# Kernel tuning notes

Hardware: AMD Instinct MI355X
Metric: run time of the kernel (lower is better)

The kernel has to match this reference:

```python
import jax, jax.numpy as jnp
import numpy as np

STRIDE = 1
PADDING = 1  # zeros padding mode

def setup_inputs() -> dict:
    key = jax.random.key(0)
    k1, k2, k3 = jax.random.split(key, 3)
    N, C_in, H, W = 32, 128, 56, 56
    C_out, kH, kW = 256, 3, 3
    x = jax.random.normal(k1, (N, C_in, H, W), dtype=jnp.float32)
    fan_in = C_in * kH * kW
    weight = jax.random.normal(k2, (C_out, C_in, kH, kW), dtype=jnp.float32) / np.sqrt(fan_in)
    bias = jax.random.normal(k3, (C_out,), dtype=jnp.float32) * 0.01
    return {"x": x, "weight": weight, "bias": bias}

def reference(x, weight, bias):
    # Same math as the im2col unfold + GEMM: a standard 2D cross-correlation
    # with zero padding. Expressed as the fused implicit-GEMM conv primitive.
    out = jax.lax.conv_general_dilated(
        x, weight,
        window_strides=(STRIDE, STRIDE),
        padding=[(PADDING, PADDING), (PADDING, PADDING)],
        dimension_numbers=("NCHW", "OIHW", "NCHW"),
    )
    # bias broadcast over (N, C_out, H_out, W_out)
    return out + bias[None, :, None, None]
```

## Files before the change

### kernel.cpp

```cpp
#include <hip/hip_runtime.h>


typedef __attribute__((ext_vector_type(8))) short short8;
typedef __attribute__((ext_vector_type(4))) float float4v;

constexpr int NB = 32, CI = 128, HH = 56, WW = 56, CO = 256;
constexpr int HWP = HH * WW;
constexpr int HP = 58, WP = 58;
constexpr size_t XTP_BYTES = (size_t)NB * HP * WP * CI * 2;
constexpr size_t WT_OFF    = XTP_BYTES;
constexpr size_t WT_BYTES  = (size_t)9 * CO * CI * 2;
constexpr size_t WS_NEED   = WT_OFF + WT_BYTES;

__device__ inline ushort f2bf(float v) {
    union { float f; uint u; } c; c.f = v;
    uint u = c.u;
    return (ushort)((u + 0x7fffu + ((u >> 16) & 1u)) >> 16);
}

__device__ inline void gll(const ushort* g, ushort* l) {
    __builtin_amdgcn_global_load_lds(
        (const __attribute__((address_space(1))) uint*)g,
        (__attribute__((address_space(3))) uint*)l, 16, 0, 0);
}

__global__ __launch_bounds__(256) void xform_x(const float* __restrict__ x,
                                               ushort* __restrict__ xTp) {
    int b = blockIdx.x;
    int cit = b & 3;
    int hwt = (b >> 2) % 49;
    int n   = b / (4 * 49);
    int ci0 = cit * 32, hw0 = hwt * 64;
    __shared__ float t[32][65];
    int tx = threadIdx.x;
    int col = tx & 63, r4 = tx >> 6;
#pragma unroll
    for (int rr = 0; rr < 8; ++rr) {
        int row = rr * 4 + r4;
        t[row][col] = x[((size_t)n * CI + ci0 + row) * HWP + hw0 + col];
    }
    __syncthreads();
    int i = tx & 31, j0 = tx >> 5;
#pragma unroll
    for (int jj = 0; jj < 8; ++jj) {
        int j = jj * 8 + j0;
        int hw = hw0 + j;
        int h = hw / WW, w = hw % WW;
        xTp[(((size_t)n * HP + h + 1) * WP + (w + 1)) * CI + ci0 + i] = f2bf(t[i][j]);
    }
}

__global__ __launch_bounds__(256) void xform_border(ushort* __restrict__ xTp) {
    int u = blockIdx.x * 256 + threadIdx.x;
    int ci8 = u & 15;
    int r = u >> 4;
    int n = r / 228, bb = r % 228;
    int hp, wp;
    if (bb < 58)       { hp = 0;  wp = bb; }
    else if (bb < 116) { hp = 57; wp = bb - 58; }
    else { int c = bb - 116; hp = 1 + (c >> 1); wp = (c & 1) * 57; }
    short8 z = (short8)0;
    *reinterpret_cast<short8*>(xTp + (((size_t)n * HP + hp) * WP + wp) * CI + ci8 * 8) = z;
}

__global__ __launch_bounds__(256) void xform_w(const float* __restrict__ w,
                                               ushort* __restrict__ wT) {
    int o = blockIdx.x * 256 + threadIdx.x;
    int ci = o & 127;
    int co = (o >> 7) & 255;
    int tap = o >> 15;
    wT[o] = f2bf(w[((size_t)co * CI + ci) * 9 + tap]);
}

__global__ __launch_bounds__(256, 3) void gemm_conv(
    const ushort* __restrict__ xTp, const ushort* __restrict__ wT,
    const float* __restrict__ bias, float* __restrict__ out)
{
    __shared__ ushort As[2][64 * 64];
    __shared__ ushort Bs[2][128 * 64];

    int b = blockIdx.x;
    int logical = (b & 7) * 392 + (b >> 3);
    const int cblk = logical & 3;
    const int mblk = logical >> 2;

    const int tid = threadIdx.x, lane = tid & 63, wv = tid >> 6;
    const int wr = wv >> 1;
    const int wc = wv & 1;

    const int s8 = (((tid & 7) ^ ((tid >> 3) & 7))) * 8;
    const int rowL = tid >> 3;
    const int dstB = rowL * 64 + (tid & 7) * 8;

    int aOff[2];
#pragma unroll
    for (int p = 0; p < 2; ++p)
        aOff[p] = (cblk * 64 + p * 32 + rowL) * CI + s8;
    int bPix[4];
#pragma unroll
    for (int p = 0; p < 4; ++p) {
        int m = mblk * 128 + p * 32 + rowL;
        int n = m / HWP, hw = m % HWP, h = hw / WW, w = hw % WW;
        bPix[p] = ((n * HP + h + 1) * WP + (w + 1)) * CI + s8;
    }

    const int ck0 = (((lane >> 4)) ^ (lane & 7)) * 8;
    const int ck1 = ((4 + (lane >> 4)) ^ (lane & 7)) * 8;
    const int aRowOff = (wr * 32 + (lane & 15)) * 64;
    const int bRowOff = (wc * 64 + (lane & 15)) * 64;

    float4v acc[2][4];
#pragma unroll
    for (int i = 0; i < 2; ++i)
#pragma unroll
        for (int j = 0; j < 4; ++j) acc[i][j] = (float4v)(0.0f);

    auto STAGE = [&](int buf, int t) {
        int tap = t >> 1, kh = (t & 1) * 64;
        int ao = tap * (CO * CI) + kh;
        ushort* asb = &As[buf][0];
#pragma unroll
        for (int p = 0; p < 2; ++p)
            gll(wT + aOff[p] + ao, asb + p * 2048 + dstB);
        int dh = tap / 3 - 1, dw = tap % 3 - 1;
        int bo = (dh * WP + dw) * CI + kh;
        ushort* bsb = &Bs[buf][0];
#pragma unroll
        for (int p = 0; p < 4; ++p)
            gll(xTp + bPix[p] + bo, bsb + p * 2048 + dstB);
    };

    auto COMPUTE = [&](int buf) {
        const ushort* asb = &As[buf][0];
        const ushort* bsb = &Bs[buf][0];
        short8 aF[2][2], bF[4][2];
#pragma unroll
        for (int fi = 0; fi < 2; ++fi) {
            aF[fi][0] = *(const short8*)(asb + aRowOff + fi * 1024 + ck0);
            aF[fi][1] = *(const short8*)(asb + aRowOff + fi * 1024 + ck1);
        }
#pragma unroll
        for (int gi = 0; gi < 4; ++gi) {
            bF[gi][0] = *(const short8*)(bsb + bRowOff + gi * 1024 + ck0);
            bF[gi][1] = *(const short8*)(bsb + bRowOff + gi * 1024 + ck1);
        }
        __builtin_amdgcn_s_setprio(1);
#pragma unroll
        for (int kc = 0; kc < 2; ++kc)
#pragma unroll
            for (int fi = 0; fi < 2; ++fi)
#pragma unroll
                for (int gi = 0; gi < 4; ++gi)
                    acc[fi][gi] = __builtin_amdgcn_mfma_f32_16x16x32_bf16(
                        aF[fi][kc], bF[gi][kc], acc[fi][gi], 0, 0, 0);
        __builtin_amdgcn_s_setprio(0);
    };

    STAGE(0, 0);
    __syncthreads();
#pragma unroll 1
    for (int t = 0; t < 18; ++t) {
        const int cur = t & 1;
        if (t + 1 < 18) STAGE(cur ^ 1, t + 1);
        COMPUTE(cur);
        __syncthreads();
    }

    const int co0 = cblk * 64 + wr * 32;
    const int m0  = mblk * 128 + wc * 64;
    float bv[2][4];
#pragma unroll
    for (int f = 0; f < 2; ++f)
#pragma unroll
        for (int r = 0; r < 4; ++r)
            bv[f][r] = bias[co0 + f * 16 + (lane >> 4) * 4 + r];
#pragma unroll
    for (int g = 0; g < 4; ++g) {
        int m = m0 + g * 16 + (lane & 15);
        int n = m / HWP, hw = m % HWP;
        float* obase = out + (size_t)n * CO * HWP + hw;
#pragma unroll
        for (int f = 0; f < 2; ++f) {
            int co = co0 + f * 16 + (lane >> 4) * 4;
#pragma unroll
            for (int r = 0; r < 4; ++r)
                obase[(size_t)(co + r) * HWP] = acc[f][g][r] + bv[f][r];
        }
    }
}

__global__ __launch_bounds__(256) void conv_k(
    const float* __restrict__ x, const float* __restrict__ wgt,
    const float* __restrict__ bias, float* __restrict__ out)
{
    int idx = blockIdx.x * 256 + threadIdx.x;
    int wg = idx % 14; int t = idx / 14;
    int ho = t % 56; t /= 56;
    int cog = t % 64; int n = t / 64;
    int w0 = wg * 4, co0 = cog * 4;
    float acc[4][4];
#pragma unroll
    for (int j = 0; j < 4; ++j) {
        float bj = bias[co0 + j];
#pragma unroll
        for (int p = 0; p < 4; ++p) acc[j][p] = bj;
    }
    const float* xn = x + (size_t)n * CI * HWP;
    for (int ci = 0; ci < CI; ++ci) {
        float xr[3][6];
#pragma unroll
        for (int kh = 0; kh < 3; ++kh) {
            int hi = ho + kh - 1;
            if (hi >= 0 && hi < HH) {
                const float* row = xn + ((size_t)ci * HH + hi) * WW;
                float4 cc = *reinterpret_cast<const float4*>(row + w0);
                xr[kh][1] = cc.x; xr[kh][2] = cc.y; xr[kh][3] = cc.z; xr[kh][4] = cc.w;
                xr[kh][0] = (w0 > 0) ? row[w0 - 1] : 0.0f;
                xr[kh][5] = (w0 + 4 < WW) ? row[w0 + 4] : 0.0f;
            } else {
#pragma unroll
                for (int q = 0; q < 6; ++q) xr[kh][q] = 0.0f;
            }
        }
#pragma unroll
        for (int j = 0; j < 4; ++j) {
            const float* wp = wgt + ((size_t)(co0 + j) * CI + ci) * 9;
            float wvv[9];
#pragma unroll
            for (int q = 0; q < 9; ++q) wvv[q] = wp[q];
#pragma unroll
            for (int kh = 0; kh < 3; ++kh)
#pragma unroll
                for (int kw = 0; kw < 3; ++kw)
#pragma unroll
                    for (int p = 0; p < 4; ++p)
                        acc[j][p] = fmaf(xr[kh][p + kw], wvv[kh * 3 + kw], acc[j][p]);
        }
    }
#pragma unroll
    for (int j = 0; j < 4; ++j) {
        float4 v = make_float4(acc[j][0], acc[j][1], acc[j][2], acc[j][3]);
        *reinterpret_cast<float4*>(out + (((size_t)n * CO + co0 + j) * HH + ho) * WW + w0) = v;
    }
}

extern "C" void kernel_launch(void* const* d_in, const int* in_sizes, int n_in,
                              void* d_out, int out_size, void* d_ws, size_t ws_size,
                              hipStream_t stream) {
    const float* x = (const float*)d_in[0];
    const float* w = (const float*)d_in[1];
    const float* b = (const float*)d_in[2];
    float* out = (float*)d_out;

    if (ws_size < WS_NEED) {
        hipLaunchKernelGGL(conv_k, dim3(6272), dim3(256), 0, stream, x, w, b, out);
        return;
    }

    ushort* xTp = (ushort*)d_ws;
    ushort* wT  = (ushort*)((char*)d_ws + WT_OFF);

    hipLaunchKernelGGL(xform_x, dim3(32 * 49 * 4), dim3(256), 0, stream, x, xTp);
    hipLaunchKernelGGL(xform_border, dim3(456), dim3(256), 0, stream, xTp);
    hipLaunchKernelGGL(xform_w, dim3(9 * CO * CI / 256), dim3(256), 0, stream, w, wT);
    hipLaunchKernelGGL(gemm_conv, dim3(3136), dim3(256), 0, stream,
                       xTp, wT, b, out);
}
```

Baseline: 103.3 us.

## Enlarge GEMM block tile to 128x128 with K-step 32 and new swizzle

Changes the implicit-GEMM conv block tile from 64 output channels by 128 pixels to 128 by 128, halving the grid and the K step per stage to 32 with 36 iterations. Each wave now holds a 4x4 grid of MFMA accumulators, which raises arithmetic intensity and reduces redundant loads of the input tiles. The LDS layout and XOR swizzle are redone for 128-byte rows. The costs are more accumulator registers, which may cut occupancy under launch_bounds(256,3), twice as many barriers per block, and fewer blocks to spread across CUs.

```diff
diff --git a/kernel.cpp b/kernel.cpp
--- a/kernel.cpp
+++ b/kernel.cpp
@@ -76,101 +76,92 @@
     const ushort* __restrict__ xTp, const ushort* __restrict__ wT,
     const float* __restrict__ bias, float* __restrict__ out)
 {
-    __shared__ ushort As[2][64 * 64];
-    __shared__ ushort Bs[2][128 * 64];
+    __shared__ ushort As[2][32 * 128];
+    __shared__ ushort Bs[2][32 * 128];
 
     int b = blockIdx.x;
-    int logical = (b & 7) * 392 + (b >> 3);
-    const int cblk = logical & 3;
-    const int mblk = logical >> 2;
+    int logical = (b & 7) * 196 + (b >> 3);
+    const int cblk = logical & 1;
+    const int mblk = logical >> 1;
 
     const int tid = threadIdx.x, lane = tid & 63, wv = tid >> 6;
     const int wr = wv >> 1;
     const int wc = wv & 1;
 
-    const int s8 = (((tid & 7) ^ ((tid >> 3) & 7))) * 8;
-    const int rowL = tid >> 3;
-    const int dstB = rowL * 64 + (tid & 7) * 8;
-
-    int aOff[2];
-#pragma unroll
-    for (int p = 0; p < 2; ++p)
-        aOff[p] = (cblk * 64 + p * 32 + rowL) * CI + s8;
-    int bPix[4];
-#pragma unroll
-    for (int p = 0; p < 4; ++p) {
-        int m = mblk * 128 + p * 32 + rowL;
+    int aOff[2], bPix[2];
+#pragma unroll
+    for (int p = 0; p < 2; ++p) {
+        int lr = (tid >> 4) + p * 16;
+        int q  = (tid & 15) ^ (lr & 15);
+        int tr = lr * 4 + (q >> 2);
+        int kc8 = (q & 3) * 8;
+        aOff[p] = (cblk * 128 + tr) * CI + kc8;
+        int m = mblk * 128 + tr;
         int n = m / HWP, hw = m % HWP, h = hw / WW, w = hw % WW;
-        bPix[p] = ((n * HP + h + 1) * WP + (w + 1)) * CI + s8;
-    }
-
-    const int ck0 = (((lane >> 4)) ^ (lane & 7)) * 8;
-    const int ck1 = ((4 + (lane >> 4)) ^ (lane & 7)) * 8;
-    const int aRowOff = (wr * 32 + (lane & 15)) * 64;
-    const int bRowOff = (wc * 64 + (lane & 15)) * 64;
-
-    float4v acc[2][4];
-#pragma unroll
-    for (int i = 0; i < 2; ++i)
+        bPix[p] = ((n * HP + h + 1) * WP + (w + 1)) * CI + kc8;
+    }
+    const int dstE = (tid >> 4) * 128 + (tid & 15) * 8;
+
+    const int ln = lane & 15, ch = lane >> 4;
+    int aAd[4], bAd[4];
+#pragma unroll
+    for (int f = 0; f < 4; ++f) {
+        int lrA = wr * 16 + f * 4 + (ln >> 2);
+        aAd[f] = lrA * 128 + ((((ln & 3) * 4 + ch) ^ (lrA & 15)) * 8);
+        int lrB = wc * 16 + f * 4 + (ln >> 2);
+        bAd[f] = lrB * 128 + ((((ln & 3) * 4 + ch) ^ (lrB & 15)) * 8);
+    }
+
+    float4v acc[4][4];
+#pragma unroll
+    for (int i = 0; i < 4; ++i)
 #pragma unroll
         for (int j = 0; j < 4; ++j) acc[i][j] = (float4v)(0.0f);
 
     auto STAGE = [&](int buf, int t) {
-        int tap = t >> 1, kh = (t & 1) * 64;
-        int ao = tap * (CO * CI) + kh;
-        ushort* asb = &As[buf][0];
-#pragma unroll
-        for (int p = 0; p < 2; ++p)
-            gll(wT + aOff[p] + ao, asb + p * 2048 + dstB);
+        int tap = t >> 2, kq = (t & 3) * 32;
+        int ao = tap * (CO * CI) + kq;
         int dh = tap / 3 - 1, dw = tap % 3 - 1;
-        int bo = (dh * WP + dw) * CI + kh;
-        ushort* bsb = &Bs[buf][0];
-#pragma unroll
-        for (int p = 0; p < 4; ++p)
-            gll(xTp + bPix[p] + bo, bsb + p * 2048 + dstB);
+        int bo = (dh * WP + dw) * CI + kq;
+#pragma unroll
+        for (int p = 0; p < 2; ++p) {
+            gll(wT + aOff[p] + ao, &As[buf][dstE + p * 2048]);
+            gll(xTp + bPix[p] + bo, &Bs[buf][dstE + p * 2048]);
+        }
     };
 
     auto COMPUTE = [&](int buf) {
-        const ushort* asb = &As[buf][0];
-        const ushort* bsb = &Bs[buf][0];
-        short8 aF[2][2], bF[4][2];
-#pragma unroll
-        for (int fi = 0; fi < 2; ++fi) {
-            aF[fi][0] = *(const short8*)(asb + aRowOff + fi * 1024 + ck0);
-            aF[fi][1] = *(const short8*)(asb + aRowOff + fi * 1024 + ck1);
-        }
-#pragma unroll
-        for (int gi = 0; gi < 4; ++gi) {
-            bF[gi][0] = *(const short8*)(bsb + bRowOff + gi * 1024 + ck0);
-            bF[gi][1] = *(const short8*)(bsb + bRowOff + gi * 1024 + ck1);
+        short8 aF[4], bF[4];
+#pragma unroll
+        for (int f = 0; f < 4; ++f) {
+            aF[f] = *(const short8*)(&As[buf][aAd[f]]);
+            bF[f] = *(const short8*)(&Bs[buf][bAd[f]]);
         }
         __builtin_amdgcn_s_setprio(1);
 #pragma unroll
-        for (int kc = 0; kc < 2; ++kc)
-#pragma unroll
-            for (int fi = 0; fi < 2; ++fi)
-#pragma unroll
-                for (int gi = 0; gi < 4; ++gi)
-                    acc[fi][gi] = __builtin_amdgcn_mfma_f32_16x16x32_bf16(
-                        aF[fi][kc], bF[gi][kc], acc[fi][gi], 0, 0, 0);
+        for (int fi = 0; fi < 4; ++fi)
+#pragma unroll
+            for (int gi = 0; gi < 4; ++gi)
+                acc[fi][gi] = __builtin_amdgcn_mfma_f32_16x16x32_bf16(
+                    aF[fi], bF[gi], acc[fi][gi], 0, 0, 0);
         __builtin_amdgcn_s_setprio(0);
     };
 
     STAGE(0, 0);
     __syncthreads();
 #pragma unroll 1
-    for (int t = 0; t < 18; ++t) {
+    for (int t = 0; t < 36; ++t) {
         const int cur = t & 1;
-        if (t + 1 < 18) STAGE(cur ^ 1, t + 1);
+        if (t + 1 < 36) STAGE(cur ^ 1, t + 1);
         COMPUTE(cur);
         __syncthreads();
     }
 
-    const int co0 = cblk * 64 + wr * 32;
+    const int co0 = cblk * 128 + wr * 64;
     const int m0  = mblk * 128 + wc * 64;
-    float bv[2][4];
-#pragma unroll
-    for (int f = 0; f < 2; ++f)
+    float bv[4][4];
+#pragma unroll
+    for (int f = 0; f < 4; ++f)
 #pragma unroll
         for (int r = 0; r < 4; ++r)
             bv[f][r] = bias[co0 + f * 16 + (lane >> 4) * 4 + r];
@@ -180,7 +171,7 @@
         int n = m / HWP, hw = m % HWP;
         float* obase = out + (size_t)n * CO * HWP + hw;
 #pragma unroll
-        for (int f = 0; f < 2; ++f) {
+        for (int f = 0; f < 4; ++f) {
             int co = co0 + f * 16 + (lane >> 4) * 4;
 #pragma unroll
             for (int r = 0; r < 4; ++r)
@@ -263,6 +254,6 @@
     hipLaunchKernelGGL(xform_x, dim3(32 * 49 * 4), dim3(256), 0, stream, x, xTp);
     hipLaunchKernelGGL(xform_border, dim3(456), dim3(256), 0, stream, xTp);
     hipLaunchKernelGGL(xform_w, dim3(9 * CO * CI / 256), dim3(256), 0, stream, w, wT);
-    hipLaunchKernelGGL(gemm_conv, dim3(3136), dim3(256), 0, stream,
+    hipLaunchKernelGGL(gemm_conv, dim3(1568), dim3(256), 0, stream,
                        xTp, wT, b, out);
 }
```

Result: slower. 110.9 us (+7.4%).
